# Performance work log

Measured on AMD Instinct MI355X. Metric: run time of the kernel, lower is better.

The kernel has to match this reference:

```python
import jax, jax.numpy as jnp
import numpy as np

NEG = -1e30  # finite stand-in for -inf in the sparse-softmax mask


def setup_inputs() -> dict:
    key = jax.random.key(0)
    kh, kwl, kwn, kn = jax.random.split(key, 4)
    B, S, D, E = 8, 4096, 1024, 64
    return {
        "h": jax.random.normal(kh, (B, S, D), dtype=jnp.float32),
        "Wl": jax.random.normal(kwl, (E, D), dtype=jnp.float32) * 0.02,
        "bl": jnp.zeros((E,), dtype=jnp.float32),
        "Wn": jax.random.normal(kwn, (E, D), dtype=jnp.float32) * 0.02,
        "bn": jnp.zeros((E,), dtype=jnp.float32),
        "noise": jax.random.normal(kn, (B, S, E), dtype=jnp.float32),
        "top_k": 2,
    }


def reference(h, Wl, bl, Wn, bn, noise, top_k):
    # logits, noise std: two small linears over the expert dim
    logits = jnp.einsum("bsd,ed->bse", h, Wl) + bl          # [B,S,E]
    std = jax.nn.softplus(jnp.einsum("bsd,ed->bse", h, Wn) + bn)
    noisy = logits + noise * std                              # [B,S,E]

    full_p = jax.nn.softmax(noisy, axis=-1)

    topk_vals, ix = jax.lax.top_k(noisy, top_k)               # [B,S,k]
    E = noisy.shape[-1]
    # scatter top-k values back into a -inf-filled tensor == mask non-topk
    mask = jax.nn.one_hot(ix, E, dtype=jnp.bool_).any(axis=-2)  # [B,S,E]
    sparse = jnp.where(mask, noisy, NEG)
    route_p = jax.nn.softmax(sparse, axis=-1)
    return route_p, ix, full_p
```

## Files before the change

### kernel.cpp

```cpp
#include <hip/hip_runtime.h>
#include <math.h>


#define DIM 1024
#define NEXP 64
#define CS 132
#define LOSCALE 2048.0f
#define INV_LOSCALE (1.0f / 2048.0f)

using half8v   = __attribute__((ext_vector_type(8)))  _Float16;
using floatx16 = __attribute__((ext_vector_type(16))) float;

#define MFMA32(a, b, c) __builtin_amdgcn_mfma_f32_32x32x16_f16((a), (b), (c), 0, 0, 0)

__device__ inline void gll16(const void* g, void* l) {
    __builtin_amdgcn_global_load_lds(
        (const __attribute__((address_space(1))) unsigned int*)g,
        (__attribute__((address_space(3))) unsigned int*)l, 16, 0, 0);
}

__global__ __launch_bounds__(512)
void prep_B(const float* __restrict__ Wl, const float* __restrict__ Wn,
            _Float16* __restrict__ Bp)
{
    const int idx = blockIdx.x * 512 + threadIdx.x;
    const int r  = idx >> 7;
    const int c2 = idx & 127;
    const float* W = (r < 64) ? (Wl + (size_t)r * DIM) : (Wn + (size_t)(r - 64) * DIM);
    float f[8];
    *(float4*)(f)     = *(const float4*)(W + c2 * 8);
    *(float4*)(f + 4) = *(const float4*)(W + c2 * 8 + 4);
    half8v hi, lo;
#pragma unroll
    for (int i = 0; i < 8; i++) {
        _Float16 hh = (_Float16)f[i];
        hi[i] = hh;
        lo[i] = (_Float16)((f[i] - (float)hh) * LOSCALE);
    }
    const int t = c2 >> 2, cf = c2 & 3, sw = r & 7;
    _Float16* base = Bp + ((size_t)t * 128 + r) * 64;
    *(half8v*)(base + ((cf ^ sw) << 3))      = hi;
    *(half8v*)(base + (((4 | cf) ^ sw) << 3)) = lo;
}

__global__ __launch_bounds__(512, 4)
void router_fused(const float* __restrict__ h, const _Float16* __restrict__ Bp,
                  const float* __restrict__ bl, const float* __restrict__ bn,
                  const float* __restrict__ noise,
                  float* __restrict__ outR, float* __restrict__ outIx,
                  float* __restrict__ outF)
{
    __shared__ __align__(16) char lds_raw[49152];

    const int tid   = threadIdx.x;
    const int wv    = tid >> 6;
    const int lane  = tid & 63;
    const int row31 = lane & 31;
    const int oct   = lane >> 5;
    const int tokg  = (wv >> 2) * 32;
    const int expg  = (wv & 3) * 32;
    const int tok0  = blockIdx.x * 64;

    const int rS = tid >> 3, cS = tid & 7;
    const float*    aSrc = h + (size_t)(tok0 + rS) * DIM + ((cS ^ (rS & 7)) << 2);
    const _Float16* bSrc = Bp + (size_t)tid * 8;
    char* dA = lds_raw + (tid << 4);
    char* dB = lds_raw + 16384 + (tid << 4);

#define ISSUE(tt, sel) do { \
        gll16(aSrc + (tt) * 32,                  dA + (sel) * 8192);        \
        gll16(bSrc + (size_t)(tt) * 8192,        dB + (sel) * 16384);       \
        gll16(bSrc + (size_t)(tt) * 8192 + 4096, dB + (sel) * 16384 + 8192);\
    } while (0)

    const int rA = tokg + row31, rB = expg + row31;
    const int swA = (rA & 7) << 4, swB = (rB & 7) << 4;
    const char* A0p = lds_raw + rA * 128;
    const char* A1p = A0p + 8192;
    const char* B0p = lds_raw + 16384 + rB * 128;
    const char* B1p = B0p + 16384;
    const int a00 = (oct * 32) ^ swA,      a01 = (oct * 32 + 16) ^ swA;
    const int a10 = (64 + oct * 32) ^ swA, a11 = (64 + oct * 32 + 16) ^ swA;
    const int bh0 = (oct * 16) ^ swB,      bh1 = (32 + oct * 16) ^ swB;
    const int bl0 = (64 + oct * 16) ^ swB, bl1 = (96 + oct * 16) ^ swB;

    floatx16 acc1, acc2;
#pragma unroll
    for (int i = 0; i < 16; i++) { acc1[i] = 0.f; acc2[i] = 0.f; }

    ISSUE(0, 0);
    ISSUE(1, 1);
    __syncthreads();

#pragma unroll 2
    for (int t = 0; t < 32; t++) {
        const char* Ab = (t & 1) ? A1p : A0p;
        const char* Bb = (t & 1) ? B1p : B0p;
#pragma unroll
        for (int ks = 0; ks < 2; ks++) {
            const float4 f0 = *(const float4*)(Ab + (ks ? a10 : a00));
            const float4 f1 = *(const float4*)(Ab + (ks ? a11 : a01));
            const half8v bH = *(const half8v*)(Bb + (ks ? bh1 : bh0));
            const half8v bL = *(const half8v*)(Bb + (ks ? bl1 : bl0));
            float f[8] = {f0.x, f0.y, f0.z, f0.w, f1.x, f1.y, f1.z, f1.w};
            half8v aH, aL;
#pragma unroll
            for (int i = 0; i < 8; i++) {
                _Float16 hh = (_Float16)f[i];
                aH[i] = hh;
                aL[i] = (_Float16)((f[i] - (float)hh) * LOSCALE);
            }
            acc1 = MFMA32(aH, bH, acc1);
            acc2 = MFMA32(aH, bL, acc2);
            acc2 = MFMA32(aL, bH, acc2);
        }
        __syncthreads();
        if (t < 30) ISSUE(t + 2, t & 1);
    }
#undef ISSUE

    float* Cs = (float*)lds_raw;
#pragma unroll
    for (int i = 0; i < 16; i++) {
        int rowt = (i & 3) + 8 * (i >> 2) + 4 * oct;
        Cs[(tokg + rowt) * CS + expg + row31] = acc1[i] + acc2[i] * INV_LOSCALE;
    }
    __syncthreads();

    const float blv = bl[lane];
    const float bnv = bn[lane];

    for (int t = wv; t < 64; t += 8) {
        const int gt = tok0 + t;
        float xr = Cs[t * CS + lane] + blv;
        float xf = Cs[t * CS + 64 + lane] + bnv;
        float nz = noise[(size_t)gt * NEXP + lane];

        float stdv = fmaxf(xf, 0.f) + log1pf(expf(-fabsf(xf)));
        float noisy = fmaf(nz, stdv, xr);

        float m = noisy;
#pragma unroll
        for (int o = 32; o > 0; o >>= 1) m = fmaxf(m, __shfl_xor(m, o, 64));
        float p = expf(noisy - m);
        float s = p;
#pragma unroll
        for (int o = 32; o > 0; o >>= 1) s += __shfl_xor(s, o, 64);
        float fullp = p / s;

        float v = noisy; int idx = lane;
#pragma unroll
        for (int o = 32; o > 0; o >>= 1) {
            float ov = __shfl_xor(v, o, 64);
            int   oi = __shfl_xor(idx, o, 64);
            if (ov > v || (ov == v && oi < idx)) { v = ov; idx = oi; }
        }
        const float v1 = v; const int i1 = idx;
        v = (lane == i1) ? -INFINITY : noisy; idx = lane;
#pragma unroll
        for (int o = 32; o > 0; o >>= 1) {
            float ov = __shfl_xor(v, o, 64);
            int   oi = __shfl_xor(idx, o, 64);
            if (ov > v || (ov == v && oi < idx)) { v = ov; idx = oi; }
        }
        const float v2 = v; const int i2 = idx;

        float e2 = expf(v2 - v1);
        float den = 1.f + e2;
        float routep = (lane == i1) ? (1.f / den) : ((lane == i2) ? (e2 / den) : 0.f);

        outR[(size_t)gt * NEXP + lane] = routep;
        outF[(size_t)gt * NEXP + lane] = fullp;
        if (lane == 0) {
            outIx[(size_t)gt * 2 + 0] = (float)i1;
            outIx[(size_t)gt * 2 + 1] = (float)i2;
        }
    }
}

extern "C" void kernel_launch(void* const* d_in, const int* in_sizes, int n_in,
                              void* d_out, int out_size, void* d_ws, size_t ws_size,
                              hipStream_t stream) {
    const float* h     = (const float*)d_in[0];
    const float* Wl    = (const float*)d_in[1];
    const float* bl    = (const float*)d_in[2];
    const float* Wn    = (const float*)d_in[3];
    const float* bn    = (const float*)d_in[4];
    const float* noise = (const float*)d_in[5];
    float* out = (float*)d_out;

    const int M = in_sizes[0] / DIM;
    float* outR  = out;
    float* outIx = out + (size_t)M * NEXP;
    float* outF  = outIx + (size_t)M * 2;

    _Float16* Bp = (_Float16*)d_ws;

    prep_B<<<32, 512, 0, stream>>>(Wl, Wn, Bp);
    router_fused<<<M / 64, 512, 0, stream>>>(h, Bp, bl, bn, noise, outR, outIx, outF);
}
```

Before: 243.6 us.

## Split h to fp16 hi/lo once per tile in LDS, 256-thread blocks

The kernel now loads h through registers and converts each element to fp16 hi/lo exactly once, storing both halves in LDS. Before, each of the four expert-group waves reconverted the same fp32 tile. Blocks shrink to 4 waves, each computing two 32x32 token tiles against its expert slice, which doubles the reuse of the B fragment. The row max for the full softmax is now taken from the top-1 reduction, dropping one shuffle reduction. The cost is more registers (four accumulators) and register-staged loads instead of direct global-to-LDS copies, which may lower occupancy or latency hiding.

```diff
diff --git a/kernel.cpp b/kernel.cpp
--- a/kernel.cpp
+++ b/kernel.cpp
@@ -7,6 +7,8 @@
 #define CS 132
 #define LOSCALE 2048.0f
 #define INV_LOSCALE (1.0f / 2048.0f)
+#define ABUF 8192
+#define BUFSZ 24576
 
 using half8v   = __attribute__((ext_vector_type(8)))  _Float16;
 using floatx16 = __attribute__((ext_vector_type(16))) float;
@@ -39,98 +41,122 @@
     }
     const int t = c2 >> 2, cf = c2 & 3, sw = r & 7;
     _Float16* base = Bp + ((size_t)t * 128 + r) * 64;
-    *(half8v*)(base + ((cf ^ sw) << 3))      = hi;
+    *(half8v*)(base + ((cf ^ sw) << 3))       = hi;
     *(half8v*)(base + (((4 | cf) ^ sw) << 3)) = lo;
 }
 
-__global__ __launch_bounds__(512, 4)
+__global__ __launch_bounds__(256, 3)
 void router_fused(const float* __restrict__ h, const _Float16* __restrict__ Bp,
                   const float* __restrict__ bl, const float* __restrict__ bn,
                   const float* __restrict__ noise,
                   float* __restrict__ outR, float* __restrict__ outIx,
                   float* __restrict__ outF)
 {
-    __shared__ __align__(16) char lds_raw[49152];
+    __shared__ __align__(16) char lds_raw[2 * BUFSZ];
 
     const int tid   = threadIdx.x;
     const int wv    = tid >> 6;
     const int lane  = tid & 63;
     const int row31 = lane & 31;
     const int oct   = lane >> 5;
-    const int tokg  = (wv >> 2) * 32;
-    const int expg  = (wv & 3) * 32;
+    const int expg  = wv * 32;
     const int tok0  = blockIdx.x * 64;
 
-    const int rS = tid >> 3, cS = tid & 7;
-    const float*    aSrc = h + (size_t)(tok0 + rS) * DIM + ((cS ^ (rS & 7)) << 2);
-    const _Float16* bSrc = Bp + (size_t)tid * 8;
-    char* dA = lds_raw + (tid << 4);
-    char* dB = lds_raw + 16384 + (tid << 4);
-
-#define ISSUE(tt, sel) do { \
-        gll16(aSrc + (tt) * 32,                  dA + (sel) * 8192);        \
-        gll16(bSrc + (size_t)(tt) * 8192,        dB + (sel) * 16384);       \
-        gll16(bSrc + (size_t)(tt) * 8192 + 4096, dB + (sel) * 16384 + 8192);\
+    const int rS = tid >> 2, gS = tid & 3;
+    const float* aSrc = h + (size_t)(tok0 + rS) * DIM + gS * 8;
+    const int aWrow = rS * 128;
+    const int wHi = ((gS ^ (rS & 7)) << 4);
+    const int wLo = (((4 | gS) ^ (rS & 7)) << 4);
+
+    const _Float16* bSrc = Bp + tid * 8;
+    char* dB = lds_raw + ABUF + (tid << 4);
+
+    const int rowA0 = row31 * 128;
+    const int rowA1 = rowA0 + 32 * 128;
+    const int rowB  = ABUF + (expg + row31) * 128;
+    const int swA = (row31 & 7) << 4;
+    const int swB = ((expg + row31) & 7) << 4;
+
+    floatx16 acc1_0, acc2_0, acc1_1, acc2_1;
+#pragma unroll
+    for (int i = 0; i < 16; i++) { acc1_0[i] = 0.f; acc2_0[i] = 0.f;
+                                   acc1_1[i] = 0.f; acc2_1[i] = 0.f; }
+
+#define CVTW(dst) do {                                                         \
+        float f_[8] = {a0v.x, a0v.y, a0v.z, a0v.w, a1v.x, a1v.y, a1v.z, a1v.w};\
+        half8v hi_, lo_;                                                       \
+        _Pragma("unroll")                                                      \
+        for (int i_ = 0; i_ < 8; i_++) {                                       \
+            _Float16 hh_ = (_Float16)f_[i_];                                   \
+            hi_[i_] = hh_;                                                     \
+            lo_[i_] = (_Float16)((f_[i_] - (float)hh_) * LOSCALE);             \
+        }                                                                      \
+        *(half8v*)((dst) + aWrow + wHi) = hi_;                                 \
+        *(half8v*)((dst) + aWrow + wLo) = lo_;                                 \
     } while (0)
 
-    const int rA = tokg + row31, rB = expg + row31;
-    const int swA = (rA & 7) << 4, swB = (rB & 7) << 4;
-    const char* A0p = lds_raw + rA * 128;
-    const char* A1p = A0p + 8192;
-    const char* B0p = lds_raw + 16384 + rB * 128;
-    const char* B1p = B0p + 16384;
-    const int a00 = (oct * 32) ^ swA,      a01 = (oct * 32 + 16) ^ swA;
-    const int a10 = (64 + oct * 32) ^ swA, a11 = (64 + oct * 32 + 16) ^ swA;
-    const int bh0 = (oct * 16) ^ swB,      bh1 = (32 + oct * 16) ^ swB;
-    const int bl0 = (64 + oct * 16) ^ swB, bl1 = (96 + oct * 16) ^ swB;
-
-    floatx16 acc1, acc2;
-#pragma unroll
-    for (int i = 0; i < 16; i++) { acc1[i] = 0.f; acc2[i] = 0.f; }
-
-    ISSUE(0, 0);
-    ISSUE(1, 1);
+#define ISSUE_B(tt) do {                                                       \
+        char* db_ = dB + ((tt) & 1) * BUFSZ;                                   \
+        const _Float16* bs_ = bSrc + (size_t)(tt) * 8192;                      \
+        gll16(bs_,        db_);                                                \
+        gll16(bs_ + 2048, db_ + 4096);                                         \
+        gll16(bs_ + 4096, db_ + 8192);                                         \
+        gll16(bs_ + 6144, db_ + 12288);                                        \
+    } while (0)
+
+    float4 a0v = *(const float4*)(aSrc);
+    float4 a1v = *(const float4*)(aSrc + 4);
+    ISSUE_B(0);
+    CVTW(lds_raw);
+    a0v = *(const float4*)(aSrc + 32);
+    a1v = *(const float4*)(aSrc + 36);
     __syncthreads();
 
-#pragma unroll 2
     for (int t = 0; t < 32; t++) {
-        const char* Ab = (t & 1) ? A1p : A0p;
-        const char* Bb = (t & 1) ? B1p : B0p;
+        char* nbuf = lds_raw + ((t + 1) & 1) * BUFSZ;
+        if (t < 31) {
+            CVTW(nbuf);
+            ISSUE_B(t + 1);
+        }
+        if (t < 30) {
+            a0v = *(const float4*)(aSrc + 32 * (t + 2));
+            a1v = *(const float4*)(aSrc + 32 * (t + 2) + 4);
+        }
+        const char* base = lds_raw + (t & 1) * BUFSZ;
 #pragma unroll
         for (int ks = 0; ks < 2; ks++) {
-            const float4 f0 = *(const float4*)(Ab + (ks ? a10 : a00));
-            const float4 f1 = *(const float4*)(Ab + (ks ? a11 : a01));
-            const half8v bH = *(const half8v*)(Bb + (ks ? bh1 : bh0));
-            const half8v bL = *(const half8v*)(Bb + (ks ? bl1 : bl0));
-            float f[8] = {f0.x, f0.y, f0.z, f0.w, f1.x, f1.y, f1.z, f1.w};
-            half8v aH, aL;
-#pragma unroll
-            for (int i = 0; i < 8; i++) {
-                _Float16 hh = (_Float16)f[i];
-                aH[i] = hh;
-                aL[i] = (_Float16)((f[i] - (float)hh) * LOSCALE);
-            }
-            acc1 = MFMA32(aH, bH, acc1);
-            acc2 = MFMA32(aH, bL, acc2);
-            acc2 = MFMA32(aL, bH, acc2);
+            const int hc = (ks * 2 + oct) << 4;
+            const half8v aH0 = *(const half8v*)(base + rowA0 + (hc ^ swA));
+            const half8v aL0 = *(const half8v*)(base + rowA0 + ((64 | hc) ^ swA));
+            const half8v aH1 = *(const half8v*)(base + rowA1 + (hc ^ swA));
+            const half8v aL1 = *(const half8v*)(base + rowA1 + ((64 | hc) ^ swA));
+            const half8v bH  = *(const half8v*)(base + rowB + (hc ^ swB));
+            const half8v bL  = *(const half8v*)(base + rowB + ((64 | hc) ^ swB));
+            acc1_0 = MFMA32(aH0, bH, acc1_0);
+            acc2_0 = MFMA32(aH0, bL, acc2_0);
+            acc2_0 = MFMA32(aL0, bH, acc2_0);
+            acc1_1 = MFMA32(aH1, bH, acc1_1);
+            acc2_1 = MFMA32(aH1, bL, acc2_1);
+            acc2_1 = MFMA32(aL1, bH, acc2_1);
         }
         __syncthreads();
-        if (t < 30) ISSUE(t + 2, t & 1);
-    }
-#undef ISSUE
+    }
+#undef ISSUE_B
+#undef CVTW
 
     float* Cs = (float*)lds_raw;
 #pragma unroll
     for (int i = 0; i < 16; i++) {
-        int rowt = (i & 3) + 8 * (i >> 2) + 4 * oct;
-        Cs[(tokg + rowt) * CS + expg + row31] = acc1[i] + acc2[i] * INV_LOSCALE;
+        const int rowt = (i & 3) + 8 * (i >> 2) + 4 * oct;
+        Cs[rowt * CS + expg + row31]        = acc1_0[i] + acc2_0[i] * INV_LOSCALE;
+        Cs[(32 + rowt) * CS + expg + row31] = acc1_1[i] + acc2_1[i] * INV_LOSCALE;
     }
     __syncthreads();
 
     const float blv = bl[lane];
     const float bnv = bn[lane];
 
-    for (int t = wv; t < 64; t += 8) {
+    for (int t = wv; t < 64; t += 4) {
         const int gt = tok0 + t;
         float xr = Cs[t * CS + lane] + blv;
         float xf = Cs[t * CS + 64 + lane] + bnv;
@@ -139,15 +165,6 @@
         float stdv = fmaxf(xf, 0.f) + log1pf(expf(-fabsf(xf)));
         float noisy = fmaf(nz, stdv, xr);
 
-        float m = noisy;
-#pragma unroll
-        for (int o = 32; o > 0; o >>= 1) m = fmaxf(m, __shfl_xor(m, o, 64));
-        float p = expf(noisy - m);
-        float s = p;
-#pragma unroll
-        for (int o = 32; o > 0; o >>= 1) s += __shfl_xor(s, o, 64);
-        float fullp = p / s;
-
         float v = noisy; int idx = lane;
 #pragma unroll
         for (int o = 32; o > 0; o >>= 1) {
@@ -156,6 +173,13 @@
             if (ov > v || (ov == v && oi < idx)) { v = ov; idx = oi; }
         }
         const float v1 = v; const int i1 = idx;
+
+        float p = expf(noisy - v1);
+        float s = p;
+#pragma unroll
+        for (int o = 32; o > 0; o >>= 1) s += __shfl_xor(s, o, 64);
+        float fullp = p / s;
+
         v = (lane == i1) ? -INFINITY : noisy; idx = lane;
 #pragma unroll
         for (int o = 32; o > 0; o >>= 1) {
@@ -197,5 +221,5 @@
     _Float16* Bp = (_Float16*)d_ws;
 
     prep_B<<<32, 512, 0, stream>>>(Wl, Wn, Bp);
-    router_fused<<<M / 64, 512, 0, stream>>>(h, Bp, bl, bn, noise, outR, outIx, outF);
-}
+    router_fused<<<M / 64, 256, 0, stream>>>(h, Bp, bl, bn, noise, outR, outIx, outF);
+}
```

New measurement: 256.6 us. +5.3%, slower.

## Replace LDS-staged GEMM with direct register-prefetched global loads per wave

Applied to the files above, without the earlier changes.

Removes the global_load_lds double-buffered staging of h and B tiles, so each wave loads its A and B MFMA fragments straight from global memory into registers with a two-step software prefetch. Blocks shrink to 32 tokens and 4 waves, each wave covering 32 expert columns, and the B layout is repacked so the hi and lo halves sit next to each other for each lane. It also drops the separate max reduction for the full softmax by reusing the top-1 value as the max. The aim is to remove LDS traffic and per-iteration barriers. In exchange, h fragment loads are now strided, partly uncoalesced global reads, and the B matrix is re-read by many more blocks.

```diff
diff --git a/kernel.cpp b/kernel.cpp
--- a/kernel.cpp
+++ b/kernel.cpp
@@ -12,12 +12,6 @@
 using floatx16 = __attribute__((ext_vector_type(16))) float;
 
 #define MFMA32(a, b, c) __builtin_amdgcn_mfma_f32_32x32x16_f16((a), (b), (c), 0, 0, 0)
-
-__device__ inline void gll16(const void* g, void* l) {
-    __builtin_amdgcn_global_load_lds(
-        (const __attribute__((address_space(1))) unsigned int*)g,
-        (__attribute__((address_space(3))) unsigned int*)l, 16, 0, 0);
-}
 
 __global__ __launch_bounds__(512)
 void prep_B(const float* __restrict__ Wl, const float* __restrict__ Wn,
@@ -37,100 +31,89 @@
         hi[i] = hh;
         lo[i] = (_Float16)((f[i] - (float)hh) * LOSCALE);
     }
-    const int t = c2 >> 2, cf = c2 & 3, sw = r & 7;
-    _Float16* base = Bp + ((size_t)t * 128 + r) * 64;
-    *(half8v*)(base + ((cf ^ sw) << 3))      = hi;
-    *(half8v*)(base + (((4 | cf) ^ sw) << 3)) = lo;
+    const int t = c2 >> 1, hf = c2 & 1;
+    _Float16* base = Bp + ((size_t)t * 128 + r) * 32 + hf * 16;
+    *(half8v*)(base)     = hi;
+    *(half8v*)(base + 8) = lo;
 }
 
-__global__ __launch_bounds__(512, 4)
+__global__ __launch_bounds__(256, 4)
 void router_fused(const float* __restrict__ h, const _Float16* __restrict__ Bp,
                   const float* __restrict__ bl, const float* __restrict__ bn,
                   const float* __restrict__ noise,
                   float* __restrict__ outR, float* __restrict__ outIx,
                   float* __restrict__ outF)
 {
-    __shared__ __align__(16) char lds_raw[49152];
+    __shared__ float Cs[32 * CS];
 
     const int tid   = threadIdx.x;
     const int wv    = tid >> 6;
     const int lane  = tid & 63;
     const int row31 = lane & 31;
     const int oct   = lane >> 5;
-    const int tokg  = (wv >> 2) * 32;
-    const int expg  = (wv & 3) * 32;
-    const int tok0  = blockIdx.x * 64;
+    const int colb  = wv * 32;
+    const int tok0  = blockIdx.x * 32;
 
-    const int rS = tid >> 3, cS = tid & 7;
-    const float*    aSrc = h + (size_t)(tok0 + rS) * DIM + ((cS ^ (rS & 7)) << 2);
-    const _Float16* bSrc = Bp + (size_t)tid * 8;
-    char* dA = lds_raw + (tid << 4);
-    char* dB = lds_raw + 16384 + (tid << 4);
-
-#define ISSUE(tt, sel) do { \
-        gll16(aSrc + (tt) * 32,                  dA + (sel) * 8192);        \
-        gll16(bSrc + (size_t)(tt) * 8192,        dB + (sel) * 16384);       \
-        gll16(bSrc + (size_t)(tt) * 8192 + 4096, dB + (sel) * 16384 + 8192);\
-    } while (0)
-
-    const int rA = tokg + row31, rB = expg + row31;
-    const int swA = (rA & 7) << 4, swB = (rB & 7) << 4;
-    const char* A0p = lds_raw + rA * 128;
-    const char* A1p = A0p + 8192;
-    const char* B0p = lds_raw + 16384 + rB * 128;
-    const char* B1p = B0p + 16384;
-    const int a00 = (oct * 32) ^ swA,      a01 = (oct * 32 + 16) ^ swA;
-    const int a10 = (64 + oct * 32) ^ swA, a11 = (64 + oct * 32 + 16) ^ swA;
-    const int bh0 = (oct * 16) ^ swB,      bh1 = (32 + oct * 16) ^ swB;
-    const int bl0 = (64 + oct * 16) ^ swB, bl1 = (96 + oct * 16) ^ swB;
+    const float*    aP = h  + (size_t)(tok0 + row31) * DIM + oct * 8;
+    const _Float16* bP = Bp + (size_t)(colb + row31) * 32 + oct * 16;
 
     floatx16 acc1, acc2;
 #pragma unroll
     for (int i = 0; i < 16; i++) { acc1[i] = 0.f; acc2[i] = 0.f; }
 
-    ISSUE(0, 0);
-    ISSUE(1, 1);
-    __syncthreads();
+#define LOADA(s, A0, A1) do {                                                  \
+        (A0) = *(const float4*)(aP + (s) * 16);                                \
+        (A1) = *(const float4*)(aP + (s) * 16 + 4);                            \
+    } while (0)
+#define LOADB(s, BH, BL) do {                                                  \
+        (BH) = *(const half8v*)(bP + (size_t)(s) * 4096);                      \
+        (BL) = *(const half8v*)(bP + (size_t)(s) * 4096 + 8);                  \
+    } while (0)
+#define STEP(A0, A1, BH, BL) do {                                              \
+        float f_[8] = {(A0).x, (A0).y, (A0).z, (A0).w,                         \
+                       (A1).x, (A1).y, (A1).z, (A1).w};                        \
+        half8v aH_, aL_;                                                       \
+        _Pragma("unroll")                                                      \
+        for (int i_ = 0; i_ < 8; i_++) {                                       \
+            _Float16 hh_ = (_Float16)f_[i_];                                   \
+            aH_[i_] = hh_;                                                     \
+            aL_[i_] = (_Float16)((f_[i_] - (float)hh_) * LOSCALE);             \
+        }                                                                      \
+        acc1 = MFMA32(aH_, (BH), acc1);                                        \
+        acc2 = MFMA32(aH_, (BL), acc2);                                        \
+        acc2 = MFMA32(aL_, (BH), acc2);                                        \
+    } while (0)
 
-#pragma unroll 2
-    for (int t = 0; t < 32; t++) {
-        const char* Ab = (t & 1) ? A1p : A0p;
-        const char* Bb = (t & 1) ? B1p : B0p;
-#pragma unroll
-        for (int ks = 0; ks < 2; ks++) {
-            const float4 f0 = *(const float4*)(Ab + (ks ? a10 : a00));
-            const float4 f1 = *(const float4*)(Ab + (ks ? a11 : a01));
-            const half8v bH = *(const half8v*)(Bb + (ks ? bh1 : bh0));
-            const half8v bL = *(const half8v*)(Bb + (ks ? bl1 : bl0));
-            float f[8] = {f0.x, f0.y, f0.z, f0.w, f1.x, f1.y, f1.z, f1.w};
-            half8v aH, aL;
-#pragma unroll
-            for (int i = 0; i < 8; i++) {
-                _Float16 hh = (_Float16)f[i];
-                aH[i] = hh;
-                aL[i] = (_Float16)((f[i] - (float)hh) * LOSCALE);
-            }
-            acc1 = MFMA32(aH, bH, acc1);
-            acc2 = MFMA32(aH, bL, acc2);
-            acc2 = MFMA32(aL, bH, acc2);
-        }
-        __syncthreads();
-        if (t < 30) ISSUE(t + 2, t & 1);
+    float4 aE0, aE1, aO0, aO1;
+    half8v bHE, bLE, bHO, bLO;
+    LOADA(0, aE0, aE1); LOADB(0, bHE, bLE);
+    LOADA(1, aO0, aO1); LOADB(1, bHO, bLO);
+
+    for (int tb = 0; tb < 31; ++tb) {
+        const int s = 2 * tb;
+        STEP(aE0, aE1, bHE, bLE);
+        LOADA(s + 2, aE0, aE1); LOADB(s + 2, bHE, bLE);
+        STEP(aO0, aO1, bHO, bLO);
+        LOADA(s + 3, aO0, aO1); LOADB(s + 3, bHO, bLO);
     }
-#undef ISSUE
+    STEP(aE0, aE1, bHE, bLE);
+    STEP(aO0, aO1, bHO, bLO);
 
-    float* Cs = (float*)lds_raw;
+#undef STEP
+#undef LOADB
+#undef LOADA
+
 #pragma unroll
     for (int i = 0; i < 16; i++) {
-        int rowt = (i & 3) + 8 * (i >> 2) + 4 * oct;
-        Cs[(tokg + rowt) * CS + expg + row31] = acc1[i] + acc2[i] * INV_LOSCALE;
+        const int rowt = (i & 3) + 8 * (i >> 2) + 4 * oct;
+        Cs[rowt * CS + colb + row31] = acc1[i] + acc2[i] * INV_LOSCALE;
     }
     __syncthreads();
 
     const float blv = bl[lane];
     const float bnv = bn[lane];
 
-    for (int t = wv; t < 64; t += 8) {
+    for (int t = wv; t < 32; t += 4) {
         const int gt = tok0 + t;
         float xr = Cs[t * CS + lane] + blv;
         float xf = Cs[t * CS + 64 + lane] + bnv;
@@ -138,15 +121,6 @@
 
         float stdv = fmaxf(xf, 0.f) + log1pf(expf(-fabsf(xf)));
         float noisy = fmaf(nz, stdv, xr);
-
-        float m = noisy;
-#pragma unroll
-        for (int o = 32; o > 0; o >>= 1) m = fmaxf(m, __shfl_xor(m, o, 64));
-        float p = expf(noisy - m);
-        float s = p;
-#pragma unroll
-        for (int o = 32; o > 0; o >>= 1) s += __shfl_xor(s, o, 64);
-        float fullp = p / s;
 
         float v = noisy; int idx = lane;
 #pragma unroll
@@ -156,6 +130,13 @@
             if (ov > v || (ov == v && oi < idx)) { v = ov; idx = oi; }
         }
         const float v1 = v; const int i1 = idx;
+
+        float p = expf(noisy - v1);
+        float s = p;
+#pragma unroll
+        for (int o = 32; o > 0; o >>= 1) s += __shfl_xor(s, o, 64);
+        float fullp = p / s;
+
         v = (lane == i1) ? -INFINITY : noisy; idx = lane;
 #pragma unroll
         for (int o = 32; o > 0; o >>= 1) {
@@ -197,5 +178,5 @@
     _Float16* Bp = (_Float16*)d_ws;
 
     prep_B<<<32, 512, 0, stream>>>(Wl, Wn, Bp);
-    router_fused<<<M / 64, 512, 0, stream>>>(h, Bp, bl, bn, noise, outR, outIx, outF);
+    router_fused<<<M / 32, 256, 0, stream>>>(h, Bp, bl, bn, noise, outR, outIx, outF);
 }
```

After: 293.3 us. 20.4% more time.
